# Kernel tuning notes

Hardware: AMD Instinct MI355X
Metric: run time of the kernel (lower is better)

Reference implementation:

```python
import jax, jax.numpy as jnp
import numpy as np

B, T, I, O = 128, 512, 700, 128  # batch, nb_steps, input_size, output_size
TIME_STEP, TAU_SYN, TAU_MEM, GAMMA_SHAPE = 1e-3, 10e-3, 20e-3, 3.0


def setup_inputs() -> dict:
    key = jax.random.key(0)
    k1, k2 = jax.random.split(key)
    inputs = jax.random.normal(k1, (B, T, I), dtype=jnp.float32)
    bound = 1.0 / np.sqrt(I)  # kaiming-uniform-like fan_in bound
    w = jax.random.uniform(k2, (I, O), minval=-bound, maxval=bound, dtype=jnp.float32)
    # heterogeneous per-neuron decay constants (het_ab=True), frozen params
    rng = np.random.default_rng(0)
    alpha = jnp.asarray(np.exp(-TIME_STEP / rng.gamma(GAMMA_SHAPE, TAU_SYN / GAMMA_SHAPE, (1, O))), dtype=jnp.float32)
    beta = jnp.asarray(np.exp(-TIME_STEP / rng.gamma(GAMMA_SHAPE, TAU_MEM / GAMMA_SHAPE, (1, O))), dtype=jnp.float32)
    return {"inputs": inputs, "w": w, "alpha": alpha, "beta": beta}


def reference(inputs, w, alpha, beta):
    # h: (B, T, O)
    h = jnp.einsum('btc,cd->btd', inputs, w)
    Bh, Th, Oh = h.shape
    zeros = jnp.zeros((Bh, Oh), dtype=h.dtype)
    one_minus_beta = 1.0 - beta  # beta is frozen, detach is a no-op here

    def step(carry, ht):
        syn, mem = carry
        new_syn = alpha * syn + ht
        new_mem = beta * mem + one_minus_beta * syn  # uses OLD syn
        return (new_syn, new_mem), (new_syn, new_mem)

    # scan over the first T-1 timesteps (time-major)
    h_tm = jnp.swapaxes(h[:, :Th - 1], 0, 1)  # (T-1, B, O)
    _, (syn_seq, mem_seq) = jax.lax.scan(step, (zeros, zeros), h_tm)
    syn_rec = jnp.concatenate([zeros[:, None], jnp.swapaxes(syn_seq, 0, 1)], axis=1)  # (B, T, O)
    mem_rec = jnp.concatenate([zeros[:, None], jnp.swapaxes(mem_seq, 0, 1)], axis=1)
    return (syn_rec, mem_rec)
```

## Files before the change

kernel.cpp:

```cpp
#include <hip/hip_runtime.h>
#include <hip/hip_bf16.h>
#include <stdint.h>

#define Bsz 128
#define Tn  512
#define In  700
#define On  128
#define Mn  (Bsz * Tn)
#define KP  704
#define NSEG 16
#define LSEG 32
#define BO   (Bsz * On)
#define NKT  22

using bf16x8 = __attribute__((ext_vector_type(8))) short;
using f32x4  = __attribute__((ext_vector_type(4))) float;

__device__ __forceinline__ uint32_t f2bf(float f) {
  union { float f; uint32_t u; } v; v.f = f;
  return (v.u + 0x7fffu + ((v.u >> 16) & 1u)) >> 16;
}

__device__ __forceinline__ bf16x8 cvt8(float4 f0, float4 f1) {
  bf16x8 r;
  r[0] = (short)f2bf(f0.x); r[1] = (short)f2bf(f0.y);
  r[2] = (short)f2bf(f0.z); r[3] = (short)f2bf(f0.w);
  r[4] = (short)f2bf(f1.x); r[5] = (short)f2bf(f1.y);
  r[6] = (short)f2bf(f1.z); r[7] = (short)f2bf(f1.w);
  return r;
}

__device__ __forceinline__ void gload16(const void* g, void* l) {
  __builtin_amdgcn_global_load_lds(
      (__attribute__((address_space(1))) void*)g,
      (__attribute__((address_space(3))) void*)l, 16, 0, 0);
}

__global__ void prep_wt(const float* __restrict__ w, ushort* __restrict__ w_t) {
  int idx = blockIdx.x * 256 + threadIdx.x;
  if (idx >= On * KP) return;
  int col = idx / KP, k = idx - col * KP;
  float v = (k < In) ? w[(size_t)k * On + col] : 0.0f;
  w_t[(size_t)col * KP + k] = (ushort)f2bf(v);
}

union SMU {
  struct {
    uint32_t A[2][4096];
    uint32_t B[2][2048];
  } db;
  float sc[128 * 132];
};

__global__ __launch_bounds__(256, 2) void gemm_h(
    const float* __restrict__ A,
    const ushort* __restrict__ Wt,
    float* __restrict__ H,
    float2* __restrict__ ep,
    const float* __restrict__ alpha, const float* __restrict__ beta)
{
  __shared__ __align__(16) SMU sm;

  const int tid  = threadIdx.x;
  const int bm   = blockIdx.x;
  const int lane = tid & 63;
  const int wid  = tid >> 6;
  const int wm   = wid >> 1, wn = wid & 1;
  const int l16  = lane & 15, lkb = lane >> 4;

  f32x4 acc[4][4];
#pragma unroll
  for (int i = 0; i < 4; ++i)
#pragma unroll
    for (int n = 0; n < 4; ++n) acc[i][n] = (f32x4){0.f, 0.f, 0.f, 0.f};

  auto stage = [&](int bi, int kt) {
    const int k0 = kt * 32;
#pragma unroll
    for (int is = 0; is < 4; ++is) {
      const int q   = is * 256 + wid * 64 + lane;
      const int row = q >> 3, sl = q & 7;
      int gk = k0 + ((sl ^ (row & 7)) << 2);
      if (gk >= In) gk = k0;
      gload16(A + (size_t)(bm * 128 + row) * In + gk,
              &sm.db.A[bi][is * 1024 + wid * 256]);
    }
#pragma unroll
    for (int is = 0; is < 2; ++is) {
      const int q   = is * 256 + wid * 64 + lane;
      const int col = q >> 2, sl = q & 3;
      const int ks  = sl ^ ((col >> 1) & 3);
      gload16(Wt + (size_t)col * KP + k0 + ks * 8,
              &sm.db.B[bi][is * 1024 + wid * 256]);
    }
  };

  int cur = 0;
  stage(0, 0);
  __syncthreads();

  for (int kt = 0; kt < NKT; ++kt) {
    if (kt + 1 < NKT) stage(cur ^ 1, kt + 1);

    const float4* Af = (const float4*)sm.db.A[cur];
    const bf16x8* Bf = (const bf16x8*)sm.db.B[cur];

    bf16x8 af[4], bfr[4];
#pragma unroll
    for (int i = 0; i < 4; ++i) {
      const int row = wm * 64 + i * 16 + l16;
      const int s0  = (lkb * 2) ^ (row & 7);
      const int s1  = (lkb * 2 + 1) ^ (row & 7);
      af[i] = cvt8(Af[row * 8 + s0], Af[row * 8 + s1]);
    }
#pragma unroll
    for (int n = 0; n < 4; ++n) {
      const int col = wn * 64 + n * 16 + l16;
      bfr[n] = Bf[col * 4 + (lkb ^ ((col >> 1) & 3))];
    }
#pragma unroll
    for (int i = 0; i < 4; ++i)
#pragma unroll
      for (int n = 0; n < 4; ++n)
        acc[i][n] = __builtin_amdgcn_mfma_f32_16x16x32_bf16(af[i], bfr[n], acc[i][n], 0, 0, 0);

    __syncthreads();
    cur ^= 1;
  }

#pragma unroll
  for (int i = 0; i < 4; ++i)
#pragma unroll
    for (int n = 0; n < 4; ++n) {
      const int col = wn * 64 + n * 16 + l16;
#pragma unroll
      for (int r = 0; r < 4; ++r) {
        const int row = wm * 64 + i * 16 + lkb * 4 + r;
        sm.sc[row * 132 + col] = acc[i][n][r];
      }
    }
  __syncthreads();

  const size_t hbase = (size_t)bm * 128 * 128;
#pragma unroll
  for (int i2 = 0; i2 < 16; ++i2) {
    const int q = i2 * 256 + tid;
    const int row = q >> 5, v = q & 31;
    *(float4*)&H[hbase + row * 128 + v * 4] =
        *(const float4*)&sm.sc[row * 132 + v * 4];
  }

  if (ep) {
    const int o = tid & 127;
    const float a = alpha[o], bt = beta[o], omb = 1.0f - bt;
    const int b = bm >> 2, seg0 = (bm & 3) * 4;
#pragma unroll
    for (int cc = 0; cc < 2; ++cc) {
      const int sl = (tid >> 7) + cc * 2;
      float S = 0.f, M = 0.f;
      const float* base = &sm.sc[(sl * 32) * 132 + o];
#pragma unroll
      for (int t = 0; t < 32; ++t) {
        const float x = base[t * 132];
        M = fmaf(bt, M, omb * S);
        S = fmaf(a, S, x);
      }
      ep[(size_t)(seg0 + sl) * BO + b * On + o] = make_float2(S, M);
    }
  }
}

__global__ __launch_bounds__(256) void scan_prefix(
    float2* __restrict__ ep,
    const float* __restrict__ alpha, const float* __restrict__ beta)
{
  const int idx = blockIdx.x * 256 + threadIdx.x;
  const int o = idx & (On - 1);
  const float a = alpha[o], bt = beta[o], omb = 1.0f - bt;
  float aL = 1.f, bL = 1.f, cL = 0.f;
#pragma unroll
  for (int i = 0; i < LSEG; ++i) {
    cL = fmaf(bt, cL, omb * aL);
    aL *= a; bL *= bt;
  }
  float S = 0.f, M = 0.f;
  for (int j = 0; j < NSEG; ++j) {
    const float2 e = ep[(size_t)j * BO + idx];
    ep[(size_t)j * BO + idx] = make_float2(S, M);
    const float nS = fmaf(aL, S, e.x);
    M = fmaf(bL, M, fmaf(cL, S, e.y));
    S = nS;
  }
}

__global__ __launch_bounds__(256) void scan_seg(
    float* __restrict__ syn, float* __restrict__ mem, const float2* __restrict__ ep,
    const float* __restrict__ alpha, const float* __restrict__ beta)
{
  const int cid = blockIdx.x * 256 + threadIdx.x;
  const int o   = cid & (On - 1);
  const int bs  = cid >> 7;
  const int seg = bs & (NSEG - 1), b = bs >> 4;
  const float a = alpha[o], bt = beta[o], omb = 1.0f - bt;
  const float2 v0 = ep[(size_t)seg * BO + b * On + o];
  float S = v0.x, M = v0.y;
  float* hp = syn + ((size_t)b * Tn + seg * LSEG) * On + o;
  float* mp = mem + ((size_t)b * Tn + seg * LSEG) * On + o;
  float buf[8];
#pragma unroll
  for (int d = 0; d < 8; ++d) buf[d] = hp[d * On];
  for (int tb = 0; tb < LSEG; tb += 8) {
#pragma unroll
    for (int d = 0; d < 8; ++d) {
      const int t = tb + d;
      const float x = buf[d];
      if (t + 8 < LSEG) buf[d] = hp[(t + 8) * On];
      hp[t * On] = S;
      mp[t * On] = M;
      M = fmaf(bt, M, omb * S);
      S = fmaf(a, S, x);
    }
  }
}

__global__ __launch_bounds__(64) void scan_k(
    float* __restrict__ syn, float* __restrict__ mem,
    const float* __restrict__ alpha, const float* __restrict__ beta)
{
  const int b = blockIdx.x >> 1;
  const int o = ((blockIdx.x & 1) << 6) + threadIdx.x;
  const float a = alpha[o], bt = beta[o], omb = 1.0f - bt;
  float* hp = syn + (size_t)b * Tn * On + o;
  float* mp = mem + (size_t)b * Tn * On + o;
  float S = 0.f, M = 0.f;
  float buf[8];
#pragma unroll
  for (int d = 0; d < 8; ++d) buf[d] = hp[d * On];
  for (int tb = 0; tb < Tn; tb += 8) {
#pragma unroll
    for (int d = 0; d < 8; ++d) {
      const int t = tb + d;
      const float h_t = buf[d];
      if (t + 8 < Tn) buf[d] = hp[(t + 8) * On];
      hp[t * On] = S;
      mp[t * On] = M;
      const float nS = fmaf(a, S, h_t);
      M = fmaf(bt, M, omb * S);
      S = nS;
    }
  }
}

extern "C" void kernel_launch(void* const* d_in, const int* in_sizes, int n_in,
                              void* d_out, int out_size, void* d_ws, size_t ws_size,
                              hipStream_t stream) {
  const float* inputs = (const float*)d_in[0];
  const float* w      = (const float*)d_in[1];
  const float* alpha  = (const float*)d_in[2];
  const float* beta   = (const float*)d_in[3];

  float* syn = (float*)d_out;
  float* mem = syn + (size_t)Bsz * Tn * On;
  ushort* w_t = (ushort*)mem;

  const size_t ep_bytes = (size_t)NSEG * BO * sizeof(float2);
  float2* ep = (ws_size >= ep_bytes) ? (float2*)d_ws : nullptr;

  prep_wt<<<(On * KP + 255) / 256, 256, 0, stream>>>(w, w_t);
  gemm_h<<<Mn / 128, 256, 0, stream>>>(inputs, w_t, syn, ep, alpha, beta);

  if (ep) {
    scan_prefix<<<BO / 256, 256, 0, stream>>>(ep, alpha, beta);
    scan_seg<<<(Bsz * NSEG * On) / 256, 256, 0, stream>>>(syn, mem, ep, alpha, beta);
  } else {
    scan_k<<<Bsz * 2, 64, 0, stream>>>(syn, mem, alpha, beta);
  }
}
```

Before: 70.34 us.

## Triple-buffer GEMM K-loop with vmcnt waits and fold prefix scan into segment scan

```diff
diff --git a/kernel.cpp b/kernel.cpp
--- a/kernel.cpp
+++ b/kernel.cpp
@@ -16,6 +16,8 @@
 using bf16x8 = __attribute__((ext_vector_type(8))) short;
 using f32x4  = __attribute__((ext_vector_type(4))) float;
 
+#define WAITVM(N) asm volatile("s_waitcnt vmcnt(" #N ")" ::: "memory")
+
 __device__ __forceinline__ uint32_t f2bf(float f) {
   union { float f; uint32_t u; } v; v.f = f;
   return (v.u + 0x7fffu + ((v.u >> 16) & 1u)) >> 16;
@@ -46,8 +48,8 @@
 
 union SMU {
   struct {
-    uint32_t A[2][4096];
-    uint32_t B[2][2048];
+    uint32_t A[3][4096];
+    uint32_t B[3][2048];
   } db;
   float sc[128 * 132];
 };
@@ -68,6 +70,10 @@
   const int wm   = wid >> 1, wn = wid & 1;
   const int l16  = lane & 15, lkb = lane >> 4;
 
+  const int   o_ep = tid & 127;
+  const float a_ep = alpha[o_ep];
+  const float b_ep = beta[o_ep];
+
   f32x4 acc[4][4];
 #pragma unroll
   for (int i = 0; i < 4; ++i)
@@ -95,16 +101,10 @@
     }
   };
 
-  int cur = 0;
-  stage(0, 0);
-  __syncthreads();
-
-  for (int kt = 0; kt < NKT; ++kt) {
-    if (kt + 1 < NKT) stage(cur ^ 1, kt + 1);
-
+  auto tile = [&](int kt, int cur) {
+    __builtin_amdgcn_s_barrier();
     const float4* Af = (const float4*)sm.db.A[cur];
     const bf16x8* Bf = (const bf16x8*)sm.db.B[cur];
-
     bf16x8 af[4], bfr[4];
 #pragma unroll
     for (int i = 0; i < 4; ++i) {
@@ -118,14 +118,26 @@
       const int col = wn * 64 + n * 16 + l16;
       bfr[n] = Bf[col * 4 + (lkb ^ ((col >> 1) & 3))];
     }
+    asm volatile("s_waitcnt lgkmcnt(0)" ::: "memory");
+    __builtin_amdgcn_s_barrier();
+    if (kt + 3 < NKT) stage(cur, kt + 3);
 #pragma unroll
     for (int i = 0; i < 4; ++i)
 #pragma unroll
       for (int n = 0; n < 4; ++n)
         acc[i][n] = __builtin_amdgcn_mfma_f32_16x16x32_bf16(af[i], bfr[n], acc[i][n], 0, 0, 0);
-
-    __syncthreads();
-    cur ^= 1;
+  };
+
+  stage(0, 0); stage(1, 1); stage(2, 2);
+  {
+    int cur = 0;
+    for (int kt = 0; kt < NKT - 2; ++kt) {
+      WAITVM(12);
+      tile(kt, cur);
+      cur = (cur == 2) ? 0 : cur + 1;
+    }
+    WAITVM(6);  tile(NKT - 2, (NKT - 2) % 3);
+    WAITVM(0);  tile(NKT - 1, (NKT - 1) % 3);
   }
 
 #pragma unroll
@@ -151,45 +163,21 @@
   }
 
   if (ep) {
-    const int o = tid & 127;
-    const float a = alpha[o], bt = beta[o], omb = 1.0f - bt;
+    const float a = a_ep, bt = b_ep, omb = 1.0f - b_ep;
     const int b = bm >> 2, seg0 = (bm & 3) * 4;
 #pragma unroll
     for (int cc = 0; cc < 2; ++cc) {
       const int sl = (tid >> 7) + cc * 2;
       float S = 0.f, M = 0.f;
-      const float* base = &sm.sc[(sl * 32) * 132 + o];
+      const float* base = &sm.sc[(sl * 32) * 132 + o_ep];
 #pragma unroll
       for (int t = 0; t < 32; ++t) {
         const float x = base[t * 132];
         M = fmaf(bt, M, omb * S);
         S = fmaf(a, S, x);
       }
-      ep[(size_t)(seg0 + sl) * BO + b * On + o] = make_float2(S, M);
-    }
-  }
-}
-
-__global__ __launch_bounds__(256) void scan_prefix(
-    float2* __restrict__ ep,
-    const float* __restrict__ alpha, const float* __restrict__ beta)
-{
-  const int idx = blockIdx.x * 256 + threadIdx.x;
-  const int o = idx & (On - 1);
-  const float a = alpha[o], bt = beta[o], omb = 1.0f - bt;
-  float aL = 1.f, bL = 1.f, cL = 0.f;
-#pragma unroll
-  for (int i = 0; i < LSEG; ++i) {
-    cL = fmaf(bt, cL, omb * aL);
-    aL *= a; bL *= bt;
-  }
-  float S = 0.f, M = 0.f;
-  for (int j = 0; j < NSEG; ++j) {
-    const float2 e = ep[(size_t)j * BO + idx];
-    ep[(size_t)j * BO + idx] = make_float2(S, M);
-    const float nS = fmaf(aL, S, e.x);
-    M = fmaf(bL, M, fmaf(cL, S, e.y));
-    S = nS;
+      ep[(size_t)(seg0 + sl) * BO + b * On + o_ep] = make_float2(S, M);
+    }
   }
 }
 
@@ -202,8 +190,21 @@
   const int bs  = cid >> 7;
   const int seg = bs & (NSEG - 1), b = bs >> 4;
   const float a = alpha[o], bt = beta[o], omb = 1.0f - bt;
-  const float2 v0 = ep[(size_t)seg * BO + b * On + o];
-  float S = v0.x, M = v0.y;
+
+  float aL = 1.f, bL = 1.f, cL = 0.f;
+#pragma unroll
+  for (int i = 0; i < LSEG; ++i) {
+    cL = fmaf(bt, cL, omb * aL);
+    aL *= a; bL *= bt;
+  }
+  float S = 0.f, M = 0.f;
+  for (int j = 0; j < seg; ++j) {
+    const float2 e = ep[(size_t)j * BO + b * On + o];
+    const float nS = fmaf(aL, S, e.x);
+    M = fmaf(bL, M, fmaf(cL, S, e.y));
+    S = nS;
+  }
+
   float* hp = syn + ((size_t)b * Tn + seg * LSEG) * On + o;
   float* mp = mem + ((size_t)b * Tn + seg * LSEG) * On + o;
   float buf[8];
@@ -270,7 +271,6 @@
   gemm_h<<<Mn / 128, 256, 0, stream>>>(inputs, w_t, syn, ep, alpha, beta);
 
   if (ep) {
-    scan_prefix<<<BO / 256, 256, 0, stream>>>(ep, alpha, beta);
     scan_seg<<<(Bsz * NSEG * On) / 256, 256, 0, stream>>>(syn, mem, ep, alpha, beta);
   } else {
     scan_k<<<Bsz * 2, 64, 0, stream>>>(syn, mem, alpha, beta);
```

New measurement: 63.07 us. 10.3% less time.
